# Kernel tuning notes

Hardware: AMD Instinct MI355X
Metric: run time of the kernel (lower is better)

The kernel has to match this reference:

```python
import jax, jax.numpy as jnp
import numpy as np

N, F, E, G = 50000, 128, 1600000, 64
CH = [16, 32, 64, 128, 256]
K = 3
EPS = 1e-5


def setup_inputs() -> dict:
    key = jax.random.key(0)
    ks = jax.random.split(key, 16)
    inp = {}
    inp["x"] = jax.random.normal(ks[0], (N, F), jnp.float32)
    inp["edge_weight"] = jax.random.uniform(ks[1], (E,), jnp.float32)
    inp["edge_index"] = jax.random.randint(ks[2], (2, E), 0, N)
    inp["batch_index"] = jnp.sort(jax.random.randint(ks[3], (N,), 0, G))
    dims = [F] + CH
    i = 4
    for l in range(5):
        fi, fo = dims[l], dims[l + 1]
        inp[f"W{l+1}"] = jax.random.normal(ks[i], (K, fi, fo), jnp.float32) / np.sqrt(K * fi)
        i += 1
        inp[f"b{l+1}"] = jnp.zeros((fo,), jnp.float32)
        if l < 4:  # no BN after the 5th conv
            inp[f"g{l+1}"] = jnp.ones((fo,), jnp.float32)
            inp[f"be{l+1}"] = jnp.zeros((fo,), jnp.float32)
    inp["Wd"] = jax.random.normal(ks[i], (2 * CH[-1], 4), jnp.float32) / np.sqrt(2 * CH[-1])
    inp["bd"] = jnp.zeros((4,), jnp.float32)
    inp["num_graphs"] = G
    return inp


def _bn(h, g, b):
    m = jnp.mean(h, axis=0)
    v = jnp.mean(jnp.square(h - m), axis=0)  # biased variance (torch training mode)
    return g * (h - m) / jnp.sqrt(v + EPS) + b


def reference(x, edge_weight, W1, b1, g1, be1, W2, b2, g2, be2, W3, b3, g3, be3,
              W4, b4, g4, be4, W5, b5, Wd, bd, edge_index, batch_index, num_graphs):
    n = x.shape[0]
    row, col = edge_index[0], edge_index[1]
    # sym-normalized Laplacian, lambda_max=2 -> scaled L_hat has zero diagonal,
    # off-diagonal = -w * deg^-1/2[row] * deg^-1/2[col]
    deg = jax.ops.segment_sum(edge_weight, row, num_segments=n)
    dinv = jnp.where(deg > 0, jax.lax.rsqrt(jnp.where(deg > 0, deg, 1.0)), 0.0)
    norm = -edge_weight * dinv[row] * dinv[col]

    def prop(z):  # L_hat @ z via sparse gather/scatter over edges
        return jax.ops.segment_sum(norm[:, None] * z[col], row, num_segments=n)

    def cheb(z, W, b):  # T0=z, T1=L z, T2=2 L T1 - T0
        t1 = prop(z)
        out = z @ W[0] + t1 @ W[1]
        t2 = 2.0 * prop(t1) - z
        return out + t2 @ W[2] + b

    h = _bn(jax.nn.softplus(cheb(x, W1, b1)), g1, be1)
    h = _bn(jax.nn.softplus(cheb(h, W2, b2)), g2, be2)
    h = _bn(jax.nn.softplus(cheb(h, W3, b3)), g3, be3)
    h = _bn(jax.nn.softplus(cheb(h, W4, b4)), g4, be4)
    h = cheb(h, W5, b5)

    mx = jax.ops.segment_max(h, batch_index, num_segments=num_graphs)
    mx = jnp.where(jnp.isfinite(mx), mx, 0.0)  # guard empty segments
    cnt = jax.ops.segment_sum(jnp.ones((n,), h.dtype), batch_index, num_segments=num_graphs)
    mean = jax.ops.segment_sum(h, batch_index, num_segments=num_graphs) / jnp.maximum(cnt, 1.0)[:, None]
    pooled = jnp.concatenate([mx, mean], axis=1)  # [G, 512]
    logits = pooled @ Wd + bd
    return jax.nn.log_softmax(logits, axis=-1)
```

## Files before the change

### kernel.cpp

```cpp
#include <hip/hip_runtime.h>
#include <hip/hip_fp16.h>
#include <cmath>

#define NN 50000
#define NE 1600000
#define NG 64
#define CAP 96
#define NPART 8
#define PROWS 6250

typedef __attribute__((ext_vector_type(8))) short short8_t;
typedef __attribute__((ext_vector_type(4))) float floatx4;
typedef __attribute__((ext_vector_type(4))) unsigned short us4;
typedef __attribute__((ext_vector_type(8))) unsigned short us8;

static __device__ __forceinline__ float softplusf(float x) {
    return fmaxf(x, 0.0f) + log1pf(expf(-fabsf(x)));
}

static __device__ __forceinline__ float bf2f(unsigned short u) {
    return __uint_as_float(((unsigned)u) << 16);
}
static __device__ __forceinline__ unsigned short f2bf(float x) {
    unsigned u = __float_as_uint(x);
    unsigned t = (u >> 16) & 1u;
    return (unsigned short)((u + 0x7FFFu + t) >> 16);
}
static __device__ __forceinline__ float h2f(unsigned u) {
    __half_raw r; r.x = (unsigned short)(u & 0xFFFFu);
    return __half2float(__half(r));
}
static __device__ __forceinline__ unsigned short f2h(float x) {
    __half h = __float2half_rn(x);
    return static_cast<__half_raw>(h).x;
}

static __device__ __forceinline__ void split_bf16(float x, unsigned short& hi, unsigned short& lo) {
    unsigned u = __float_as_uint(x);
    unsigned hb = u & 0xFFFF0000u;
    hi = (unsigned short)(hb >> 16);
    float r = x - __uint_as_float(hb);
    lo = f2bf(r);
}

static __device__ __forceinline__ int lower_bound_dev(const int* __restrict__ b, int val) {
    int lo = 0, hi = NN;
    while (lo < hi) {
        int mid = (lo + hi) >> 1;
        if (b[mid] < val) lo = mid + 1; else hi = mid;
    }
    return lo;
}

__global__ __launch_bounds__(256) void k_prep(
    const float* __restrict__ W1, const float* __restrict__ W3,
    const float* __restrict__ W4, const float* __restrict__ W5,
    const int* __restrict__ batch,
    unsigned short* __restrict__ bt1h, unsigned short* __restrict__ bt1l,
    unsigned short* __restrict__ bt3h, unsigned short* __restrict__ bt3l,
    unsigned short* __restrict__ bt4h, unsigned short* __restrict__ bt4l,
    unsigned short* __restrict__ bt5h, unsigned short* __restrict__ bt5l,
    int* __restrict__ gb)
{
    const int bx = blockIdx.x;
    const int tid = threadIdx.x;
    if (bx < 24) {
        int idx = bx * 256 + tid;
        if (idx < 128 * 48) {
            int k = idx / 48, j = idx - k * 48;
            float v;
            if (j < 16)      v = W1[k * 16 + j] - W1[2 * 2048 + k * 16 + j];
            else if (j < 32) v = W1[2048 + k * 16 + (j - 16)];
            else             v = W1[2 * 2048 + k * 16 + (j - 32)];
            unsigned short h, l;
            split_bf16(v, h, l);
            bt1h[(size_t)j * 128 + k] = h;
            bt1l[(size_t)j * 128 + k] = l;
        }
    } else if (bx < 48) {
        int idx = (bx - 24) * 256 + tid;
        if (idx < 96 * 64) {
            int k = idx / 64, n = idx - k * 64;
            unsigned short h, l;
            split_bf16(W3[idx], h, l);
            bt3h[(size_t)n * 96 + k] = h;
            bt3l[(size_t)n * 96 + k] = l;
        }
    } else if (bx < 144) {
        int idx = (bx - 48) * 256 + tid;
        if (idx < 192 * 128) {
            int k = idx / 128, n = idx - k * 128;
            unsigned short h, l;
            split_bf16(W4[idx], h, l);
            bt4h[(size_t)n * 192 + k] = h;
            bt4l[(size_t)n * 192 + k] = l;
        }
    } else if (bx < 528) {
        int idx = (bx - 144) * 256 + tid;
        if (idx < 384 * 256) {
            int k = idx / 256, n = idx - k * 256;
            unsigned short h, l;
            split_bf16(W5[idx], h, l);
            bt5h[(size_t)n * 384 + k] = h;
            bt5l[(size_t)n * 384 + k] = l;
        }
    } else {
        int g = tid;
        if (g <= NG) gb[g] = (g == NG) ? NN : lower_bound_dev(batch, g);
    }
}

#define ASTR 40

__global__ __launch_bounds__(256, 2) void k_build1(
    const int* __restrict__ row, const int* __restrict__ col,
    const float* __restrict__ w,
    int* __restrict__ cnt, unsigned* __restrict__ pslots,
    const float* __restrict__ A,
    const unsigned short* __restrict__ BhiT,
    const unsigned short* __restrict__ BloT,
    unsigned short* __restrict__ C)
{
    __shared__ unsigned short Ah[128 * ASTR];
    __shared__ unsigned short Al[128 * ASTR];
    __shared__ unsigned short Bh[128 * ASTR];
    __shared__ unsigned short Bl[128 * ASTR];

    const unsigned bx = blockIdx.x;
    const int tid = threadIdx.x;
    int gemmT = -1, sid = 0;
    if (bx < 2346u) {
        if (bx % 6u == 5u) gemmT = bx / 6u;
        else sid = bx - (bx + 1u) / 6u;
    } else {
        sid = bx - 391u;
    }

    if (gemmT < 0) {
        const int part = sid & (NPART - 1);
        const int bid = sid >> 3;
        const int nb = 2048 >> 3;
        const int rlo = part * PROWS;
        const int rhi = rlo + PROWS;
        for (int e = bid * 256 + tid; e < NE; e += nb * 256) {
            int r = row[e];
            if (r >= rlo && r < rhi) {
                int k = atomicAdd(&cnt[r], 1);
                k = min(k, CAP - 1);
                pslots[(size_t)r * CAP + k] = ((unsigned)col[e] << 16) | (unsigned)f2h(w[e]);
            }
        }
        return;
    }

    const int lda = 128, ldc = 48, M = NN, K = 128, Ncol = 48;
    const int lane = tid & 63;
    const int wave = tid >> 6;
    const int wm = wave >> 1, wn = wave & 1;
    const int quad = lane >> 4, l16 = lane & 15;
    const int bm = gemmT * 128, bn = 0;
    const int srow = tid >> 1;
    const int skq  = (tid & 1) * 16;

    floatx4 acc[4][4];
#pragma unroll
    for (int i = 0; i < 4; ++i)
#pragma unroll
        for (int j = 0; j < 4; ++j) acc[i][j] = (floatx4){0.f, 0.f, 0.f, 0.f};

    for (int k0 = 0; k0 < K; k0 += 32) {
        float4 a0 = make_float4(0, 0, 0, 0), a1 = a0, a2 = a0, a3 = a0;
        const int ga = bm + srow;
        if (ga < M) {
            const float* Ap = A + (size_t)ga * lda + k0 + skq;
            a0 = *(const float4*)(Ap + 0);
            a1 = *(const float4*)(Ap + 4);
            a2 = *(const float4*)(Ap + 8);
            a3 = *(const float4*)(Ap + 12);
        }
        uint4 bh0 = make_uint4(0, 0, 0, 0), bh1 = bh0, bl0 = bh0, bl1 = bh0;
        const int gb2 = bn + srow;
        if (gb2 < Ncol) {
            const unsigned short* ph = BhiT + (size_t)gb2 * K + k0 + skq;
            const unsigned short* pl = BloT + (size_t)gb2 * K + k0 + skq;
            bh0 = *(const uint4*)(ph);
            bh1 = *(const uint4*)(ph + 8);
            bl0 = *(const uint4*)(pl);
            bl1 = *(const uint4*)(pl + 8);
        }
        __attribute__((aligned(16))) unsigned short ah[16], al[16];
        const float av[16] = {a0.x, a0.y, a0.z, a0.w, a1.x, a1.y, a1.z, a1.w,
                              a2.x, a2.y, a2.z, a2.w, a3.x, a3.y, a3.z, a3.w};
#pragma unroll
        for (int i = 0; i < 16; ++i) split_bf16(av[i], ah[i], al[i]);

        __syncthreads();
        *(uint4*)&Ah[srow * ASTR + skq]     = *(const uint4*)&ah[0];
        *(uint4*)&Ah[srow * ASTR + skq + 8] = *(const uint4*)&ah[8];
        *(uint4*)&Al[srow * ASTR + skq]     = *(const uint4*)&al[0];
        *(uint4*)&Al[srow * ASTR + skq + 8] = *(const uint4*)&al[8];
        *(uint4*)&Bh[srow * ASTR + skq]     = bh0;
        *(uint4*)&Bh[srow * ASTR + skq + 8] = bh1;
        *(uint4*)&Bl[srow * ASTR + skq]     = bl0;
        *(uint4*)&Bl[srow * ASTR + skq + 8] = bl1;
        __syncthreads();

        short8_t afh[4], afl[4], bfh[4], bfl[4];
#pragma unroll
        for (int t = 0; t < 4; ++t) {
            const int m = wm * 64 + t * 16 + l16;
            afh[t] = *(const short8_t*)&Ah[m * ASTR + quad * 8];
            afl[t] = *(const short8_t*)&Al[m * ASTR + quad * 8];
            const int n = wn * 64 + t * 16 + l16;
            bfh[t] = *(const short8_t*)&Bh[n * ASTR + quad * 8];
            bfl[t] = *(const short8_t*)&Bl[n * ASTR + quad * 8];
        }
#pragma unroll
        for (int i = 0; i < 4; ++i)
#pragma unroll
            for (int j = 0; j < 4; ++j) {
                acc[i][j] = __builtin_amdgcn_mfma_f32_16x16x32_bf16(afh[i], bfh[j], acc[i][j], 0, 0, 0);
                acc[i][j] = __builtin_amdgcn_mfma_f32_16x16x32_bf16(afh[i], bfl[j], acc[i][j], 0, 0, 0);
                acc[i][j] = __builtin_amdgcn_mfma_f32_16x16x32_bf16(afl[i], bfh[j], acc[i][j], 0, 0, 0);
            }
    }

#pragma unroll
    for (int j = 0; j < 4; ++j) {
        const int colc = bn + wn * 64 + j * 16 + l16;
        if (colc >= Ncol) continue;
#pragma unroll
        for (int i = 0; i < 4; ++i) {
#pragma unroll
            for (int r = 0; r < 4; ++r) {
                const int rowc = bm + wm * 64 + i * 16 + quad * 4 + r;
                if (rowc >= M) continue;
                C[(size_t)rowc * ldc + colc] = f2bf(acc[i][j][r]);
            }
        }
    }
}

__global__ __launch_bounds__(256) void k_degsum(const int* __restrict__ cnt,
                                                const unsigned* __restrict__ pslots,
                                                float* __restrict__ dinv) {
    int tid = threadIdx.x;
    int lane = tid & 15;
    int node = blockIdx.x * 16 + (tid >> 4);
    if (node >= NN) return;
    int e = cnt[node];
    const unsigned* base = pslots + (size_t)node * CAP;
    float s = 0.0f;
    for (int k = lane; k < e; k += 16) s += h2f(base[k]);
#pragma unroll
    for (int m = 8; m >= 1; m >>= 1) s += __shfl_xor(s, m);
    if (lane == 0) dinv[node] = (s > 0.0f) ? rsqrtf(s) : 0.0f;
}

__global__ __launch_bounds__(256) void k_repack(const int* __restrict__ cnt,
                                                unsigned* __restrict__ pslots,
                                                const float* __restrict__ dinv) {
    int tid = threadIdx.x;
    int lane = tid & 15;
    int node = blockIdx.x * 16 + (tid >> 4);
    if (node >= NN) return;
    int e = cnt[node];
    float dr = dinv[node];
    unsigned* pb = pslots + (size_t)node * CAP;
    for (int k = lane; k < e; k += 16) {
        unsigned s = pb[k];
        float wv = -h2f(s) * dr * dinv[s >> 16];
        pb[k] = (s & 0xFFFF0000u) | (unsigned)f2h(wv);
    }
}

__global__ __launch_bounds__(256, 2) void k_gemm_mfma_bf(
    const unsigned short* __restrict__ A, int lda,
    const unsigned short* __restrict__ BhiT,
    const unsigned short* __restrict__ BloT,
    unsigned short* __restrict__ C, int ldc,
    int M, int K, int Ncol,
    const float* __restrict__ bias, int act)
{
    __shared__ unsigned short Ah[128 * ASTR];
    __shared__ unsigned short Bh[128 * ASTR];
    __shared__ unsigned short Bl[128 * ASTR];

    const int tid = threadIdx.x;
    const int lane = tid & 63;
    const int wave = tid >> 6;
    const int wm = wave >> 1, wn = wave & 1;
    const int quad = lane >> 4, l16 = lane & 15;
    const int bm = blockIdx.y * 128, bn = blockIdx.x * 128;
    const int srow = tid >> 1;
    const int skq  = (tid & 1) * 16;

    floatx4 acc[4][4];
#pragma unroll
    for (int i = 0; i < 4; ++i)
#pragma unroll
        for (int j = 0; j < 4; ++j) acc[i][j] = (floatx4){0.f, 0.f, 0.f, 0.f};

    for (int k0 = 0; k0 < K; k0 += 32) {
        uint4 a0 = make_uint4(0, 0, 0, 0), a1 = a0;
        const int ga = bm + srow;
        if (ga < M) {
            const unsigned short* Ap = A + (size_t)ga * lda + k0 + skq;
            a0 = *(const uint4*)(Ap);
            a1 = *(const uint4*)(Ap + 8);
        }
        uint4 bh0 = make_uint4(0, 0, 0, 0), bh1 = bh0, bl0 = bh0, bl1 = bh0;
        const int gb = bn + srow;
        if (gb < Ncol) {
            const unsigned short* ph = BhiT + (size_t)gb * K + k0 + skq;
            const unsigned short* pl = BloT + (size_t)gb * K + k0 + skq;
            bh0 = *(const uint4*)(ph);
            bh1 = *(const uint4*)(ph + 8);
            bl0 = *(const uint4*)(pl);
            bl1 = *(const uint4*)(pl + 8);
        }
        __syncthreads();
        *(uint4*)&Ah[srow * ASTR + skq]     = a0;
        *(uint4*)&Ah[srow * ASTR + skq + 8] = a1;
        *(uint4*)&Bh[srow * ASTR + skq]     = bh0;
        *(uint4*)&Bh[srow * ASTR + skq + 8] = bh1;
        *(uint4*)&Bl[srow * ASTR + skq]     = bl0;
        *(uint4*)&Bl[srow * ASTR + skq + 8] = bl1;
        __syncthreads();

        short8_t afh[4], bfh[4], bfl[4];
#pragma unroll
        for (int t = 0; t < 4; ++t) {
            const int m = wm * 64 + t * 16 + l16;
            afh[t] = *(const short8_t*)&Ah[m * ASTR + quad * 8];
            const int n = wn * 64 + t * 16 + l16;
            bfh[t] = *(const short8_t*)&Bh[n * ASTR + quad * 8];
            bfl[t] = *(const short8_t*)&Bl[n * ASTR + quad * 8];
        }
#pragma unroll
        for (int i = 0; i < 4; ++i)
#pragma unroll
            for (int j = 0; j < 4; ++j) {
                acc[i][j] = __builtin_amdgcn_mfma_f32_16x16x32_bf16(afh[i], bfh[j], acc[i][j], 0, 0, 0);
                acc[i][j] = __builtin_amdgcn_mfma_f32_16x16x32_bf16(afh[i], bfl[j], acc[i][j], 0, 0, 0);
            }
    }

#pragma unroll
    for (int j = 0; j < 4; ++j) {
        const int col = bn + wn * 64 + j * 16 + l16;
        if (col >= Ncol) continue;
        const float bv = bias ? bias[col] : 0.0f;
#pragma unroll
        for (int i = 0; i < 4; ++i) {
#pragma unroll
            for (int r = 0; r < 4; ++r) {
                const int row = bm + wm * 64 + i * 16 + quad * 4 + r;
                if (row >= M) continue;
                float v = acc[i][j][r] + bv;
                if (act) v = softplusf(v);
                C[(size_t)row * ldc + col] = f2bf(v);
            }
        }
    }
}

__global__ __launch_bounds__(256) void k_gemm(
    const unsigned short* __restrict__ A, int lda,
    const float* __restrict__ B, int ldb,
    unsigned short* __restrict__ C, int ldc,
    int M, int K, int Ncol,
    const float* __restrict__ bias, int act)
{
    __shared__ float As[16][128];
    __shared__ float Bs[16][128];
    const int tid = threadIdx.x;
    const int tx = tid & 15;
    const int ty = tid >> 4;
    const int bm = blockIdx.y * 128;
    const int bn = blockIdx.x * 128;
    const int arow = tid >> 1;
    const int akq = (tid & 1) * 8;
    const int bkr = tid >> 4;
    const int bcq = (tid & 15) * 8;

    float acc[8][8];
#pragma unroll
    for (int i = 0; i < 8; ++i)
#pragma unroll
        for (int j = 0; j < 8; ++j) acc[i][j] = 0.0f;

    for (int k0 = 0; k0 < K; k0 += 16) {
        uint4 ald = make_uint4(0, 0, 0, 0);
        int gr = bm + arow;
        if (gr < M) ald = *(const uint4*)(A + (size_t)gr * lda + k0 + akq);
        float4 b0 = make_float4(0, 0, 0, 0), b1 = make_float4(0, 0, 0, 0);
        int cb = bn + bcq;
        const float* Bp = B + (k0 + bkr) * ldb;
        if (cb < Ncol)     b0 = *(const float4*)(Bp + cb);
        if (cb + 4 < Ncol) b1 = *(const float4*)(Bp + cb + 4);
        __syncthreads();
        const unsigned short* au = (const unsigned short*)&ald;
#pragma unroll
        for (int i = 0; i < 8; ++i) As[akq + i][arow] = bf2f(au[i]);
        *(float4*)&Bs[bkr][bcq] = b0;
        *(float4*)&Bs[bkr][bcq + 4] = b1;
        __syncthreads();
#pragma unroll
        for (int kk = 0; kk < 16; ++kk) {
            float a[8], b[8];
            float4 t;
            t = *(const float4*)&As[kk][ty * 4];      a[0] = t.x; a[1] = t.y; a[2] = t.z; a[3] = t.w;
            t = *(const float4*)&As[kk][64 + ty * 4]; a[4] = t.x; a[5] = t.y; a[6] = t.z; a[7] = t.w;
            t = *(const float4*)&Bs[kk][tx * 4];      b[0] = t.x; b[1] = t.y; b[2] = t.z; b[3] = t.w;
            t = *(const float4*)&Bs[kk][64 + tx * 4]; b[4] = t.x; b[5] = t.y; b[6] = t.z; b[7] = t.w;
#pragma unroll
            for (int i = 0; i < 8; ++i)
#pragma unroll
                for (int j = 0; j < 8; ++j)
                    acc[i][j] = fmaf(a[i], b[j], acc[i][j]);
        }
    }
#pragma unroll
    for (int i = 0; i < 8; ++i) {
        int r = bm + ((i < 4) ? (ty * 4 + i) : (64 + ty * 4 + i - 4));
        if (r >= M) continue;
#pragma unroll
        for (int j = 0; j < 8; ++j) {
            int cl = bn + ((j < 4) ? (tx * 4 + j) : (64 + tx * 4 + j - 4));
            if (cl >= Ncol) continue;
            float v = acc[i][j];
            if (bias) v += bias[cl];
            if (act) v = softplusf(v);
            C[(size_t)r * ldc + cl] = f2bf(v);
        }
    }
}

__global__ __launch_bounds__(256) void k_prop(
    const int* __restrict__ cnt, const unsigned* __restrict__ pslots,
    const unsigned short* __restrict__ z, int zld, int zoff,
    unsigned short* __restrict__ out, int outld, int ooff,
    int ltw, float alpha,
    const unsigned short* __restrict__ add1, int a1ld, int a1off, float c1,
    const unsigned short* __restrict__ add2, int a2ld, int a2off,
    const float* __restrict__ bias, int act)
{
    const int T = 1 << ltw;
    const int lane = threadIdx.x & (T - 1);
    const int node = blockIdx.x * (256 >> ltw) + (threadIdx.x >> ltw);
    if (node >= NN) return;
    const int f4 = lane * 4;
    const int e = cnt[node];
    const unsigned* base = pslots + (size_t)node * CAP;
    float accA[4] = {0, 0, 0, 0};
    float accB[4] = {0, 0, 0, 0};
    const unsigned short* zp = z + zoff + f4;
    int p = 0;
    for (; p + 8 <= e; p += 8) {
        unsigned s0 = base[p + 0], s1 = base[p + 1], s2 = base[p + 2], s3 = base[p + 3];
        unsigned s4 = base[p + 4], s5 = base[p + 5], s6 = base[p + 6], s7 = base[p + 7];
        const us4 z0 = *(const us4*)(zp + (size_t)(s0 >> 16) * zld);
        const us4 z1 = *(const us4*)(zp + (size_t)(s1 >> 16) * zld);
        const us4 z2 = *(const us4*)(zp + (size_t)(s2 >> 16) * zld);
        const us4 z3 = *(const us4*)(zp + (size_t)(s3 >> 16) * zld);
        const us4 z4 = *(const us4*)(zp + (size_t)(s4 >> 16) * zld);
        const us4 z5 = *(const us4*)(zp + (size_t)(s5 >> 16) * zld);
        const us4 z6 = *(const us4*)(zp + (size_t)(s6 >> 16) * zld);
        const us4 z7 = *(const us4*)(zp + (size_t)(s7 >> 16) * zld);
        float w0 = h2f(s0), w1 = h2f(s1), w2 = h2f(s2), w3 = h2f(s3);
        float w4 = h2f(s4), w5 = h2f(s5), w6 = h2f(s6), w7 = h2f(s7);
#pragma unroll
        for (int i = 0; i < 4; ++i) {
            accA[i] = fmaf(w0, bf2f(z0[i]), accA[i]);
            accB[i] = fmaf(w1, bf2f(z1[i]), accB[i]);
            accA[i] = fmaf(w2, bf2f(z2[i]), accA[i]);
            accB[i] = fmaf(w3, bf2f(z3[i]), accB[i]);
            accA[i] = fmaf(w4, bf2f(z4[i]), accA[i]);
            accB[i] = fmaf(w5, bf2f(z5[i]), accB[i]);
            accA[i] = fmaf(w6, bf2f(z6[i]), accA[i]);
            accB[i] = fmaf(w7, bf2f(z7[i]), accB[i]);
        }
    }
    for (; p + 4 <= e; p += 4) {
        unsigned s0 = base[p + 0], s1 = base[p + 1], s2 = base[p + 2], s3 = base[p + 3];
        const us4 z0 = *(const us4*)(zp + (size_t)(s0 >> 16) * zld);
        const us4 z1 = *(const us4*)(zp + (size_t)(s1 >> 16) * zld);
        const us4 z2 = *(const us4*)(zp + (size_t)(s2 >> 16) * zld);
        const us4 z3 = *(const us4*)(zp + (size_t)(s3 >> 16) * zld);
        float w0 = h2f(s0), w1 = h2f(s1), w2 = h2f(s2), w3 = h2f(s3);
#pragma unroll
        for (int i = 0; i < 4; ++i) {
            accA[i] = fmaf(w0, bf2f(z0[i]), accA[i]);
            accB[i] = fmaf(w1, bf2f(z1[i]), accB[i]);
            accA[i] = fmaf(w2, bf2f(z2[i]), accA[i]);
            accB[i] = fmaf(w3, bf2f(z3[i]), accB[i]);
        }
    }
    for (; p < e; ++p) {
        unsigned s = base[p];
        float wv = h2f(s);
        const us4 zv = *(const us4*)(zp + (size_t)(s >> 16) * zld);
#pragma unroll
        for (int i = 0; i < 4; ++i) accA[i] = fmaf(wv, bf2f(zv[i]), accA[i]);
    }
#pragma unroll
    for (int i = 0; i < 4; ++i) accA[i] = alpha * (accA[i] + accB[i]);
    if (add1) {
        const us4 t = *(const us4*)(add1 + (size_t)node * a1ld + a1off + f4);
#pragma unroll
        for (int i = 0; i < 4; ++i) accA[i] = fmaf(c1, bf2f(t[i]), accA[i]);
    }
    if (add2) {
        const us4 t = *(const us4*)(add2 + (size_t)node * a2ld + a2off + f4);
#pragma unroll
        for (int i = 0; i < 4; ++i) accA[i] += bf2f(t[i]);
    }
    if (bias) {
        const float4 t = *(const float4*)(bias + f4);
        accA[0] += t.x; accA[1] += t.y; accA[2] += t.z; accA[3] += t.w;
    }
    if (act) {
#pragma unroll
        for (int i = 0; i < 4; ++i) accA[i] = softplusf(accA[i]);
    }
    us4 o;
#pragma unroll
    for (int i = 0; i < 4; ++i) o[i] = f2bf(accA[i]);
    *(us4*)(out + (size_t)node * outld + ooff + f4) = o;
}

__global__ __launch_bounds__(256) void k_bnstats(const unsigned short* __restrict__ h, int ld, int lc,
                                                 float* __restrict__ stats) {
    const int C = 1 << lc;
    const int tid = threadIdx.x;
    const int c = tid & (C - 1);
    const int rpb = 256 >> lc;
    int r = blockIdx.x * rpb + (tid >> lc);
    const int stride = gridDim.x * rpb;
    float s = 0.0f, q = 0.0f;
    for (; r < NN; r += stride) {
        float v = bf2f(h[(size_t)r * ld + c]);
        s += v;
        q = fmaf(v, v, q);
    }
    __shared__ float shs[256], shq[256];
    shs[tid] = s; shq[tid] = q;
    __syncthreads();
    for (int o = 128; o >= C; o >>= 1) {
        if (tid < o) { shs[tid] += shs[tid + o]; shq[tid] += shq[tid + o]; }
        __syncthreads();
    }
    if (tid < C) {
        atomicAdd(&stats[c], shs[tid]);
        atomicAdd(&stats[128 + c], shq[tid]);
    }
}

__global__ void k_bnapply(unsigned short* __restrict__ h, int ld, int lc,
                          const float* __restrict__ stats,
                          const float* __restrict__ g, const float* __restrict__ be) {
    int idx = blockIdx.x * 256 + threadIdx.x;
    const int C8 = 1 << (lc - 3);
    if (idx >= NN * C8) return;
    int r = idx >> (lc - 3);
    int c0 = (idx & (C8 - 1)) << 3;
    const float invN = 1.0f / (float)NN;
    unsigned short* hp = h + (size_t)r * ld + c0;
    us8 v = *(const us8*)hp;
    us8 o;
#pragma unroll
    for (int i = 0; i < 8; ++i) {
        int c = c0 + i;
        float m = stats[c] * invN;
        float var = fmaf(stats[128 + c], invN, -m * m);
        var = fmaxf(var, 0.0f);
        float inv = rsqrtf(var + 1e-5f);
        o[i] = f2bf(fmaf(g[c] * inv, bf2f(v[i]) - m, be[c]));
    }
    *(us8*)hp = o;
}

__global__ __launch_bounds__(256) void k_pool1(const unsigned short* __restrict__ h,
                                               const int* __restrict__ gb,
                                               float* __restrict__ partial) {
    int g = blockIdx.y;
    int j = blockIdx.x;
    int start = gb[g], end = gb[g + 1];
    int len = end - start;
    int chunk = (len + 15) >> 4;
    int s = start + j * chunk;
    int e = min(s + chunk, end);
    int c = threadIdx.x;
    float mx = -INFINITY, sum = 0.0f;
    for (int r = s; r < e; ++r) {
        float v = bf2f(h[(size_t)r * 256 + c]);
        mx = fmaxf(mx, v);
        sum += v;
    }
    size_t base = ((size_t)(g * 16 + j)) * 512;
    partial[base + c] = mx;
    partial[base + 256 + c] = sum;
}

__global__ __launch_bounds__(256) void k_pool2d(const float* __restrict__ partial,
                                                const int* __restrict__ gb,
                                                const float* __restrict__ Wd,
                                                const float* __restrict__ bd,
                                                float* __restrict__ out) {
    __shared__ float pl[512];
    __shared__ float red[4][256];
    int g = blockIdx.x;
    int c = threadIdx.x;
    float mx = -INFINITY, sum = 0.0f;
#pragma unroll
    for (int j = 0; j < 16; ++j) {
        size_t base = ((size_t)(g * 16 + j)) * 512;
        mx = fmaxf(mx, partial[base + c]);
        sum += partial[base + 256 + c];
    }
    int len = gb[g + 1] - gb[g];
    pl[c] = (len > 0) ? mx : 0.0f;
    pl[256 + c] = sum / fmaxf((float)len, 1.0f);
    __syncthreads();
    float p[4] = {0, 0, 0, 0};
    for (int k = c; k < 512; k += 256) {
        float pv = pl[k];
#pragma unroll
        for (int cc = 0; cc < 4; ++cc) p[cc] = fmaf(pv, Wd[k * 4 + cc], p[cc]);
    }
#pragma unroll
    for (int cc = 0; cc < 4; ++cc) red[cc][c] = p[cc];
    __syncthreads();
    for (int o = 128; o >= 1; o >>= 1) {
        if (c < o) {
#pragma unroll
            for (int cc = 0; cc < 4; ++cc) red[cc][c] += red[cc][c + o];
        }
        __syncthreads();
    }
    if (c == 0) {
        float l0 = red[0][0] + bd[0], l1 = red[1][0] + bd[1];
        float l2 = red[2][0] + bd[2], l3 = red[3][0] + bd[3];
        float m = fmaxf(fmaxf(l0, l1), fmaxf(l2, l3));
        float ls = m + logf(expf(l0 - m) + expf(l1 - m) + expf(l2 - m) + expf(l3 - m));
        out[g * 4 + 0] = l0 - ls;
        out[g * 4 + 1] = l1 - ls;
        out[g * 4 + 2] = l2 - ls;
        out[g * 4 + 3] = l3 - ls;
    }
}

extern "C" void kernel_launch(void* const* d_in, const int* in_sizes, int n_in,
                              void* d_out, int out_size, void* d_ws, size_t ws_size,
                              hipStream_t stream)
{
    const float* x    = (const float*)d_in[0];
    const float* ew   = (const float*)d_in[1];
    const int*   row  = (const int*)d_in[2];
    const int*   colp = row + NE;
    const int*   batch = (const int*)d_in[3];
    const float* W1 = (const float*)d_in[4];
    const float* b1 = (const float*)d_in[5];
    const float* g1 = (const float*)d_in[6];
    const float* be1 = (const float*)d_in[7];
    const float* W2 = (const float*)d_in[8];
    const float* b2 = (const float*)d_in[9];
    const float* g2 = (const float*)d_in[10];
    const float* be2 = (const float*)d_in[11];
    const float* W3 = (const float*)d_in[12];
    const float* b3 = (const float*)d_in[13];
    const float* g3 = (const float*)d_in[14];
    const float* be3 = (const float*)d_in[15];
    const float* W4 = (const float*)d_in[16];
    const float* b4 = (const float*)d_in[17];
    const float* g4 = (const float*)d_in[18];
    const float* be4 = (const float*)d_in[19];
    const float* W5 = (const float*)d_in[20];
    const float* b5 = (const float*)d_in[21];
    const float* Wd = (const float*)d_in[22];
    const float* bd = (const float*)d_in[23];
    float* outp = (float*)d_out;
    (void)in_sizes; (void)n_in; (void)out_size; (void)ws_size; (void)ew;

    char* wsb = (char*)d_ws;
    size_t off = 0;
    auto take = [&](size_t bytes) -> void* {
        void* p = wsb + off;
        off = (off + bytes + 255) & ~(size_t)255;
        return p;
    };
    int*   cnt    = (int*)take((size_t)NN * sizeof(int));
    float* dinv   = (float*)take((size_t)NN * sizeof(float));
    int*   gb     = (int*)take((NG + 1) * sizeof(int));
    unsigned* pslots = (unsigned*)take((size_t)NN * CAP * sizeof(unsigned));
    float* statsA = (float*)take(4 * 256 * sizeof(float));
    float* wcat   = (float*)take(6144 * sizeof(float));
    unsigned short* bt1h = (unsigned short*)take(48 * 128 * 2);
    unsigned short* bt1l = (unsigned short*)take(48 * 128 * 2);
    unsigned short* bt3h = (unsigned short*)take(64 * 96 * 2);
    unsigned short* bt3l = (unsigned short*)take(64 * 96 * 2);
    unsigned short* bt4h = (unsigned short*)take(128 * 192 * 2);
    unsigned short* bt4l = (unsigned short*)take(128 * 192 * 2);
    unsigned short* bt5h = (unsigned short*)take(256 * 384 * 2);
    unsigned short* bt5l = (unsigned short*)take(256 * 384 * 2);
    float* partial= (float*)take((size_t)NG * 16 * 512 * sizeof(float));
    unsigned short* P   = (unsigned short*)take((size_t)NN * 48 * 2);
    unsigned short* uv  = (unsigned short*)take((size_t)NN * 32 * 2);
    unsigned short* Hc2 = (unsigned short*)take((size_t)NN * 48 * 2);
    unsigned short* Hc3 = (unsigned short*)take((size_t)NN * 96 * 2);
    unsigned short* Hc4 = (unsigned short*)take((size_t)NN * 192 * 2);
    unsigned short* Hc5 = (unsigned short*)take((size_t)NN * 384 * 2);
    unsigned short* h5  = (unsigned short*)take((size_t)NN * 256 * 2);
    (void)wcat;

    float* stats1 = statsA;
    float* stats2 = statsA + 256;
    float* stats3 = statsA + 512;
    float* stats4 = statsA + 768;

    hipMemsetAsync(cnt, 0, NN * sizeof(int), stream);
    hipMemsetAsync(statsA, 0, 4 * 256 * sizeof(float), stream);

    k_prep<<<529, 256, 0, stream>>>(W1, W3, W4, W5, batch,
                                    bt1h, bt1l, bt3h, bt3l, bt4h, bt4l,
                                    bt5h, bt5l, gb);

    k_build1<<<2439, 256, 0, stream>>>(row, colp, ew, cnt, pslots,
                                       x, bt1h, bt1l, P);
    k_degsum<<<3125, 256, 0, stream>>>(cnt, pslots, dinv);
    k_repack<<<3125, 256, 0, stream>>>(cnt, pslots, dinv);

    k_prop<<<1563, 256, 0, stream>>>(cnt, pslots, P, 48, 16, uv, 32, 0, 3, 1.0f,
                                     nullptr, 0, 0, 0.0f, nullptr, 0, 0, nullptr, 0);
    k_prop<<<782, 256, 0, stream>>>(cnt, pslots, uv, 32, 16, Hc2, 48, 0, 2, 2.0f,
                                    P, 48, 0, 1.0f, uv, 32, 0, b1, 1);
    k_bnstats<<<256, 256, 0, stream>>>(Hc2, 48, 4, stats1);
    k_bnapply<<<391, 256, 0, stream>>>(Hc2, 48, 4, stats1, g1, be1);

    k_prop<<<782, 256, 0, stream>>>(cnt, pslots, Hc2, 48, 0, Hc2, 48, 16, 2, 1.0f,
                                    nullptr, 0, 0, 0.0f, nullptr, 0, 0, nullptr, 0);
    k_prop<<<782, 256, 0, stream>>>(cnt, pslots, Hc2, 48, 16, Hc2, 48, 32, 2, 2.0f,
                                    Hc2, 48, 0, -1.0f, nullptr, 0, 0, nullptr, 0);
    k_gemm<<<dim3(1, 391), 256, 0, stream>>>(Hc2, 48, W2, 32, Hc3, 96, NN, 48, 32, b2, 1);
    k_bnstats<<<256, 256, 0, stream>>>(Hc3, 96, 5, stats2);
    k_bnapply<<<782, 256, 0, stream>>>(Hc3, 96, 5, stats2, g2, be2);

    k_prop<<<1563, 256, 0, stream>>>(cnt, pslots, Hc3, 96, 0, Hc3, 96, 32, 3, 1.0f,
                                     nullptr, 0, 0, 0.0f, nullptr, 0, 0, nullptr, 0);
    k_prop<<<1563, 256, 0, stream>>>(cnt, pslots, Hc3, 96, 32, Hc3, 96, 64, 3, 2.0f,
                                     Hc3, 96, 0, -1.0f, nullptr, 0, 0, nullptr, 0);
    k_gemm_mfma_bf<<<dim3(1, 391), 256, 0, stream>>>(Hc3, 96, bt3h, bt3l, Hc4, 192, NN, 96, 64, b3, 1);
    k_bnstats<<<256, 256, 0, stream>>>(Hc4, 192, 6, stats3);
    k_bnapply<<<1563, 256, 0, stream>>>(Hc4, 192, 6, stats3, g3, be3);

    k_prop<<<3125, 256, 0, stream>>>(cnt, pslots, Hc4, 192, 0, Hc4, 192, 64, 4, 1.0f,
                                     nullptr, 0, 0, 0.0f, nullptr, 0, 0, nullptr, 0);
    k_prop<<<3125, 256, 0, stream>>>(cnt, pslots, Hc4, 192, 64, Hc4, 192, 128, 4, 2.0f,
                                     Hc4, 192, 0, -1.0f, nullptr, 0, 0, nullptr, 0);
    k_gemm_mfma_bf<<<dim3(1, 391), 256, 0, stream>>>(Hc4, 192, bt4h, bt4l, Hc5, 384, NN, 192, 128, b4, 1);
    k_bnstats<<<256, 256, 0, stream>>>(Hc5, 384, 7, stats4);
    k_bnapply<<<3125, 256, 0, stream>>>(Hc5, 384, 7, stats4, g4, be4);

    k_prop<<<6250, 256, 0, stream>>>(cnt, pslots, Hc5, 384, 0, Hc5, 384, 128, 5, 1.0f,
                                     nullptr, 0, 0, 0.0f, nullptr, 0, 0, nullptr, 0);
    k_prop<<<6250, 256, 0, stream>>>(cnt, pslots, Hc5, 384, 128, Hc5, 384, 256, 5, 2.0f,
                                     Hc5, 384, 0, -1.0f, nullptr, 0, 0, nullptr, 0);
    k_gemm_mfma_bf<<<dim3(2, 391), 256, 0, stream>>>(Hc5, 384, bt5h, bt5l, h5, 256, NN, 384, 256, b5, 0);

    k_pool1<<<dim3(16, 64), 256, 0, stream>>>(h5, gb, partial);
    k_pool2d<<<64, 256, 0, stream>>>(partial, gb, Wd, bd, outp);
}
```

Before: 795.5 us.

## Replace partitioned global-atomic CSR build with two-pass shared-memory bucket binning

```diff
diff --git a/kernel.cpp b/kernel.cpp
--- a/kernel.cpp
+++ b/kernel.cpp
@@ -6,8 +6,9 @@
 #define NE 1600000
 #define NG 64
 #define CAP 96
-#define NPART 8
-#define PROWS 6250
+#define BSH 7
+#define NBUCK ((NN + (1 << BSH) - 1) >> BSH)
+#define MAXBUCK 6144
 
 typedef __attribute__((ext_vector_type(8))) short short8_t;
 typedef __attribute__((ext_vector_type(4))) float floatx4;
@@ -110,55 +111,84 @@
     }
 }
 
+__global__ __launch_bounds__(256) void k_bin(const int* __restrict__ row,
+                                             const int* __restrict__ col,
+                                             const float* __restrict__ w,
+                                             int* __restrict__ bbase,
+                                             unsigned long long* __restrict__ ebuf) {
+    __shared__ int hist[NBUCK];
+    __shared__ int base[NBUCK];
+    const int t = threadIdx.x;
+    const int per = (NE + gridDim.x - 1) / gridDim.x;
+    const int e0 = blockIdx.x * per;
+    const int e1 = min(e0 + per, NE);
+    for (int i = t; i < NBUCK; i += 256) hist[i] = 0;
+    __syncthreads();
+    for (int e = e0 + t; e < e1; e += 256) atomicAdd(&hist[row[e] >> BSH], 1);
+    __syncthreads();
+    for (int i = t; i < NBUCK; i += 256) {
+        int h = hist[i];
+        base[i] = h ? atomicAdd(&bbase[i], h) : 0;
+    }
+    __syncthreads();
+    for (int i = t; i < NBUCK; i += 256) hist[i] = 0;
+    __syncthreads();
+    for (int e = e0 + t; e < e1; e += 256) {
+        int r = row[e];
+        int b = r >> BSH;
+        int k = atomicAdd(&hist[b], 1);
+        int idx = base[b] + k;
+        if (idx < MAXBUCK) {
+            unsigned pay = ((unsigned)col[e] << 16) | (unsigned)f2h(w[e]);
+            ebuf[(size_t)b * MAXBUCK + idx] =
+                ((unsigned long long)(unsigned)r << 32) | pay;
+        }
+    }
+}
+
+__global__ __launch_bounds__(256) void k_place(const int* __restrict__ bbase,
+                                               const unsigned long long* __restrict__ ebuf,
+                                               int* __restrict__ cnt,
+                                               unsigned* __restrict__ pslots) {
+    __shared__ int cl[1 << BSH];
+    const int t = threadIdx.x;
+    const int b = blockIdx.x;
+    if (t < (1 << BSH)) cl[t] = 0;
+    __syncthreads();
+    const int n = min(bbase[b], MAXBUCK);
+    const unsigned long long* eb = ebuf + (size_t)b * MAXBUCK;
+    for (int i = t; i < n; i += 256) {
+        unsigned long long pk = eb[i];
+        int r = (int)(pk >> 32);
+        int k = atomicAdd(&cl[r & ((1 << BSH) - 1)], 1);
+        k = min(k, CAP - 1);
+        pslots[(size_t)r * CAP + k] = (unsigned)pk;
+    }
+    __syncthreads();
+    int r = (b << BSH) + t;
+    if (t < (1 << BSH) && r < NN) cnt[r] = min(cl[t], CAP);
+}
+
 #define ASTR 40
 
-__global__ __launch_bounds__(256, 2) void k_build1(
-    const int* __restrict__ row, const int* __restrict__ col,
-    const float* __restrict__ w,
-    int* __restrict__ cnt, unsigned* __restrict__ pslots,
-    const float* __restrict__ A,
+__global__ __launch_bounds__(256, 2) void k_gemm_mfma_f32A(
+    const float* __restrict__ A, int lda,
     const unsigned short* __restrict__ BhiT,
     const unsigned short* __restrict__ BloT,
-    unsigned short* __restrict__ C)
+    unsigned short* __restrict__ C, int ldc,
+    int M, int K, int Ncol)
 {
     __shared__ unsigned short Ah[128 * ASTR];
     __shared__ unsigned short Al[128 * ASTR];
     __shared__ unsigned short Bh[128 * ASTR];
     __shared__ unsigned short Bl[128 * ASTR];
 
-    const unsigned bx = blockIdx.x;
     const int tid = threadIdx.x;
-    int gemmT = -1, sid = 0;
-    if (bx < 2346u) {
-        if (bx % 6u == 5u) gemmT = bx / 6u;
-        else sid = bx - (bx + 1u) / 6u;
-    } else {
-        sid = bx - 391u;
-    }
-
-    if (gemmT < 0) {
-        const int part = sid & (NPART - 1);
-        const int bid = sid >> 3;
-        const int nb = 2048 >> 3;
-        const int rlo = part * PROWS;
-        const int rhi = rlo + PROWS;
-        for (int e = bid * 256 + tid; e < NE; e += nb * 256) {
-            int r = row[e];
-            if (r >= rlo && r < rhi) {
-                int k = atomicAdd(&cnt[r], 1);
-                k = min(k, CAP - 1);
-                pslots[(size_t)r * CAP + k] = ((unsigned)col[e] << 16) | (unsigned)f2h(w[e]);
-            }
-        }
-        return;
-    }
-
-    const int lda = 128, ldc = 48, M = NN, K = 128, Ncol = 48;
     const int lane = tid & 63;
     const int wave = tid >> 6;
     const int wm = wave >> 1, wn = wave & 1;
     const int quad = lane >> 4, l16 = lane & 15;
-    const int bm = gemmT * 128, bn = 0;
+    const int bm = blockIdx.y * 128, bn = blockIdx.x * 128;
     const int srow = tid >> 1;
     const int skq  = (tid & 1) * 16;
 
@@ -712,22 +742,27 @@
     unsigned short* Hc4 = (unsigned short*)take((size_t)NN * 192 * 2);
     unsigned short* Hc5 = (unsigned short*)take((size_t)NN * 384 * 2);
     unsigned short* h5  = (unsigned short*)take((size_t)NN * 256 * 2);
+    int*   bbase  = (int*)take(NBUCK * sizeof(int));
     (void)wcat;
+    unsigned long long* ebuf = (unsigned long long*)Hc5;
 
     float* stats1 = statsA;
     float* stats2 = statsA + 256;
     float* stats3 = statsA + 512;
     float* stats4 = statsA + 768;
 
-    hipMemsetAsync(cnt, 0, NN * sizeof(int), stream);
+    hipMemsetAsync(bbase, 0, NBUCK * sizeof(int), stream);
     hipMemsetAsync(statsA, 0, 4 * 256 * sizeof(float), stream);
 
     k_prep<<<529, 256, 0, stream>>>(W1, W3, W4, W5, batch,
                                     bt1h, bt1l, bt3h, bt3l, bt4h, bt4l,
                                     bt5h, bt5l, gb);
 
-    k_build1<<<2439, 256, 0, stream>>>(row, colp, ew, cnt, pslots,
-                                       x, bt1h, bt1l, P);
+    k_bin<<<256, 256, 0, stream>>>(row, colp, ew, bbase, ebuf);
+    k_place<<<NBUCK, 256, 0, stream>>>(bbase, ebuf, cnt, pslots);
+
+    k_gemm_mfma_f32A<<<dim3(1, 391), 256, 0, stream>>>(x, 128, bt1h, bt1l, P, 48, NN, 128, 48);
+
     k_degsum<<<3125, 256, 0, stream>>>(cnt, pslots, dinv);
     k_repack<<<3125, 256, 0, stream>>>(cnt, pslots, dinv);
 
```

New measurement: 764.6 us. -3.9%, faster.
